# Optimization experiments

Hardware: AMD Instinct MI355X
Metric: run time of the kernel (lower is better)

The kernel has to match this reference:

```python
import jax, jax.numpy as jnp
import numpy as np

B, LT, LM = 4, 2048, 2048
D, F, E, H = 512, 2048, 4, 8
HD = D // H
EPS = 1e-5


def layer_norm(x, g, b):
    mu = jnp.mean(x, axis=-1, keepdims=True)
    var = jnp.mean((x - mu) ** 2, axis=-1, keepdims=True)
    return (x - mu) * jax.lax.rsqrt(var + EPS) * g + b


def mha(q_in, k_in, v_in, in_w, in_b, out_w, out_b):
    # PyTorch nn.MultiheadAttention: packed in_proj [3D, D], out_proj [D, D]
    wq, wk, wv = jnp.split(in_w, 3, axis=0)
    bq, bk, bv = jnp.split(in_b, 3)
    Bq, Lq, _ = q_in.shape
    Lk = k_in.shape[1]
    q = (q_in @ wq.T + bq).reshape(Bq, Lq, H, HD)
    k = (k_in @ wk.T + bk).reshape(Bq, Lk, H, HD)
    v = (v_in @ wv.T + bv).reshape(Bq, Lk, H, HD)
    scale = 1.0 / jnp.sqrt(jnp.asarray(HD, q.dtype))
    attn = jax.nn.softmax(jnp.einsum('bqhd,bkhd->bhqk', q, k) * scale, axis=-1)
    o = jnp.einsum('bhqk,bkhd->bqhd', attn, v).reshape(Bq, Lq, D)
    return o @ out_w.T + out_b


def moe_ff(x, gate_w, gate_b, w1, b1, w2, b2):
    # top_k == 1: argmax routing, mask-and-sum over experts (no score scaling)
    gate_scores = jax.nn.softmax(x @ gate_w.T + gate_b, axis=-1)  # [B,L,E]
    idx = jnp.argmax(gate_scores, axis=-1)                        # [B,L]
    h = jax.nn.gelu(jnp.einsum('bld,edf->eblf', x, w1) + b1[:, None, None, :], approximate=False)
    y = jnp.einsum('eblf,efd->ebld', h, w2) + b2[:, None, None, :]  # [E,B,L,D]
    onehot = jax.nn.one_hot(idx, E, dtype=x.dtype)                  # [B,L,E]
    return jnp.einsum('ebld,ble->bld', y, onehot)


def setup_inputs() -> dict:
    key = jax.random.key(0)
    ks = jax.random.split(key, 20)
    s = 0.02
    n = lambda k, shape: jax.random.normal(k, shape, jnp.float32) * s
    return {
        'x': jax.random.normal(ks[0], (B, LT, D), jnp.float32),
        'memory': jax.random.normal(ks[1], (B, LM, D), jnp.float32),
        'sa_in_w': n(ks[2], (3 * D, D)), 'sa_in_b': n(ks[3], (3 * D,)),
        'sa_out_w': n(ks[4], (D, D)), 'sa_out_b': n(ks[5], (D,)),
        'ca_in_w': n(ks[6], (3 * D, D)), 'ca_in_b': n(ks[7], (3 * D,)),
        'ca_out_w': n(ks[8], (D, D)), 'ca_out_b': n(ks[9], (D,)),
        'gate_w': n(ks[10], (E, D)), 'gate_b': n(ks[11], (E,)),
        'w1': n(ks[12], (E, D, F)), 'b1': n(ks[13], (E, F)),
        'w2': n(ks[14], (E, F, D)), 'b2': n(ks[15], (E, D)),
        'ln1_g': jnp.ones((D,), jnp.float32), 'ln1_b': jnp.zeros((D,), jnp.float32),
        'ln2_g': jnp.ones((D,), jnp.float32), 'ln2_b': jnp.zeros((D,), jnp.float32),
        'ln3_g': jnp.ones((D,), jnp.float32), 'ln3_b': jnp.zeros((D,), jnp.float32),
    }


def reference(x, memory, sa_in_w, sa_in_b, sa_out_w, sa_out_b,
              ca_in_w, ca_in_b, ca_out_w, ca_out_b,
              gate_w, gate_b, w1, b1, w2, b2,
              ln1_g, ln1_b, ln2_g, ln2_b, ln3_g, ln3_b):
    # self-attention + residual + norm (dropout is identity in eval)
    x2 = mha(x, x, x, sa_in_w, sa_in_b, sa_out_w, sa_out_b)
    x = layer_norm(x + x2, ln1_g, ln1_b)
    # cross-attention + residual + norm
    x2 = mha(x, memory, memory, ca_in_w, ca_in_b, ca_out_w, ca_out_b)
    x = layer_norm(x + x2, ln2_g, ln2_b)
    # MoE FFN + residual + norm
    x2 = moe_ff(x, gate_w, gate_b, w1, b1, w2, b2)
    x = layer_norm(x + x2, ln3_g, ln3_b)
    return x
```

## Files before the change

kernel.cpp:

```cpp
#include <hip/hip_runtime.h>

typedef unsigned short u16;
typedef __attribute__((ext_vector_type(8))) short s16x8;
typedef __attribute__((ext_vector_type(8))) unsigned short u16x8;
typedef __attribute__((ext_vector_type(4))) unsigned short u16x4;
typedef __attribute__((ext_vector_type(4))) float f32x4;

#define DEV static __device__ __forceinline__
#define MFMA __builtin_amdgcn_mfma_f32_16x16x32_bf16

DEV float bf2f(u16 u) { return __uint_as_float(((unsigned)u) << 16); }
DEV u16 f2bf(float f) {
    unsigned u = __float_as_uint(f);
    return (u16)((u + 0x7FFFu + ((u >> 16) & 1u)) >> 16);
}
DEV void split2(float v, u16& hi, u16& lo) {
    hi = f2bf(v);
    lo = f2bf(v - bf2f(hi));
}


__global__ __launch_bounds__(256) void split_k(
    const float* __restrict__ src, u16* __restrict__ dh, u16* __restrict__ dl, long n)
{
    const long i = ((long)blockIdx.x * 256 + threadIdx.x) * 8;
    if (i >= n) return;
    float4 f0 = *(const float4*)(src + i);
    float4 f1 = *(const float4*)(src + i + 4);
    float v[8] = {f0.x, f0.y, f0.z, f0.w, f1.x, f1.y, f1.z, f1.w};
    u16x8 h8, l8;
    for (int j = 0; j < 8; ++j) { u16 hh, ll; split2(v[j], hh, ll); h8[j] = hh; l8[j] = ll; }
    *(u16x8*)(dh + i) = h8;
    *(u16x8*)(dl + i) = l8;
}

__global__ __launch_bounds__(256) void splitT_k(
    const float* __restrict__ src, u16* __restrict__ dst, int K, int N)
{
    __shared__ u16 tile[64 * 72];
    const int e = blockIdx.z;
    const int n0 = blockIdx.x * 64, k0 = blockIdx.y * 64;
    const long estride = (long)K * N;
    const int tid = threadIdx.x;
    const int tr = tid >> 2, tc = (tid & 3) * 16;
    {
        const float* sp = src + e * estride + (long)(k0 + tr) * N + n0 + tc;
        for (int j = 0; j < 16; j += 4) {
            float4 f = *(const float4*)(sp + j);
            tile[tr * 72 + tc + j + 0] = f2bf(f.x);
            tile[tr * 72 + tc + j + 1] = f2bf(f.y);
            tile[tr * 72 + tc + j + 2] = f2bf(f.z);
            tile[tr * 72 + tc + j + 3] = f2bf(f.w);
        }
    }
    __syncthreads();
    {
        const int tn = tid >> 2, tk = (tid & 3) * 16;
        u16* dp = dst + e * estride + (long)(n0 + tn) * K + k0 + tk;
        u16x8 o0, o1;
        for (int j = 0; j < 8; ++j) {
            o0[j] = tile[(tk + j) * 72 + tn];
            o1[j] = tile[(tk + 8 + j) * 72 + tn];
        }
        *(u16x8*)(dp) = o0;
        *(u16x8*)(dp + 8) = o1;
    }
}

__global__ __launch_bounds__(256) void gemm_s(
    const float* __restrict__ Af, const u16* __restrict__ Ahp, const u16* __restrict__ Alp,
    int lda, int a_lo, const int* __restrict__ perm_in,
    const u16* __restrict__ Bh, const u16* __restrict__ Bl, int ldb, long b_estride,
    const int* __restrict__ tile_expert,
    const float* __restrict__ bias, int bias_estride,
    float* __restrict__ Cf, int ldcf, const int* __restrict__ perm_out,
    u16* __restrict__ Ch, long clo_off, int ldcp, int ts, long tstride,
    int K, int act)
{
    __shared__ u16 As[64 * 36], Als[64 * 36];
    __shared__ u16 Bs[64 * 36], Bls[64 * 36];
    const int mt = blockIdx.x, nt = blockIdx.y;
    int e = 0;
    if (tile_expert) { e = tile_expert[mt]; if (e < 0) return; }
    const int tid = threadIdx.x, lane = tid & 63, w = tid >> 6;
    const int wr = (w >> 1) * 32, wc = (w & 1) * 32;
    const int quad = lane >> 4, l15 = lane & 15;
    const int b_lo = (Bl != nullptr);

    const u16* Bhb = Bh + (long)e * b_estride;
    const u16* Blb = b_lo ? (Bl + (long)e * b_estride) : nullptr;

    const int r2 = tid >> 3, c4 = (tid & 7) * 4;
    const int r1 = tid >> 2, c8 = (tid & 3) * 8;
    long arow0 = 0, arow1 = 0, arowb = 0;
    bool v0 = true, v1 = true, vb = true;
    if (perm_in) {
        if (Af) {
            int p0 = perm_in[mt * 64 + r2];      v0 = p0 >= 0; arow0 = p0 < 0 ? 0 : p0;
            int p1 = perm_in[mt * 64 + r2 + 32]; v1 = p1 >= 0; arow1 = p1 < 0 ? 0 : p1;
        } else {
            int pb = perm_in[mt * 64 + r1];      vb = pb >= 0; arowb = pb < 0 ? 0 : pb;
        }
    } else {
        arow0 = (long)mt * 64 + r2; arow1 = arow0 + 32; arowb = (long)mt * 64 + r1;
    }

    f32x4 acc[2][2] = {};

    for (int k0 = 0; k0 < K; k0 += 32) {
        __syncthreads();
        if (Af) {
            for (int half = 0; half < 2; ++half) {
                const int row = half * 32 + r2;
                const long ar = half ? arow1 : arow0;
                const bool va = half ? v1 : v0;
                float4 v = va ? *(const float4*)(Af + ar * (long)lda + k0 + c4)
                              : make_float4(0.f, 0.f, 0.f, 0.f);
                float vv[4] = {v.x, v.y, v.z, v.w};
                u16x4 h4, l4;
                for (int i = 0; i < 4; ++i) { u16 hh, ll; split2(vv[i], hh, ll); h4[i] = hh; l4[i] = ll; }
                *(u16x4*)&As[row * 36 + c4] = h4;
                if (a_lo) *(u16x4*)&Als[row * 36 + c4] = l4;
            }
        } else {
            const long ao = arowb * (long)lda + k0 + c8;
            u16x8 h8 = vb ? *(const u16x8*)(Ahp + ao) : (u16x8)(u16)0;
            *(u16x8*)&As[r1 * 36 + c8] = h8;
            if (a_lo) {
                u16x8 l8 = vb ? *(const u16x8*)(Alp + ao) : (u16x8)(u16)0;
                *(u16x8*)&Als[r1 * 36 + c8] = l8;
            }
        }
        {
            const long bo = ((long)nt * 64 + r1) * ldb + k0 + c8;
            *(u16x8*)&Bs[r1 * 36 + c8] = *(const u16x8*)(Bhb + bo);
            if (b_lo) *(u16x8*)&Bls[r1 * 36 + c8] = *(const u16x8*)(Blb + bo);
        }
        __syncthreads();
        s16x8 ah0 = *(const s16x8*)&As[(wr + l15) * 36 + quad * 8];
        s16x8 ah1 = *(const s16x8*)&As[(wr + 16 + l15) * 36 + quad * 8];
        s16x8 bh0 = *(const s16x8*)&Bs[(wc + l15) * 36 + quad * 8];
        s16x8 bh1 = *(const s16x8*)&Bs[(wc + 16 + l15) * 36 + quad * 8];
        acc[0][0] = MFMA(ah0, bh0, acc[0][0], 0, 0, 0);
        acc[0][1] = MFMA(ah0, bh1, acc[0][1], 0, 0, 0);
        acc[1][0] = MFMA(ah1, bh0, acc[1][0], 0, 0, 0);
        acc[1][1] = MFMA(ah1, bh1, acc[1][1], 0, 0, 0);
        if (a_lo) {
            s16x8 al0 = *(const s16x8*)&Als[(wr + l15) * 36 + quad * 8];
            s16x8 al1 = *(const s16x8*)&Als[(wr + 16 + l15) * 36 + quad * 8];
            acc[0][0] = MFMA(al0, bh0, acc[0][0], 0, 0, 0);
            acc[0][1] = MFMA(al0, bh1, acc[0][1], 0, 0, 0);
            acc[1][0] = MFMA(al1, bh0, acc[1][0], 0, 0, 0);
            acc[1][1] = MFMA(al1, bh1, acc[1][1], 0, 0, 0);
        }
        if (b_lo) {
            s16x8 bl0 = *(const s16x8*)&Bls[(wc + l15) * 36 + quad * 8];
            s16x8 bl1 = *(const s16x8*)&Bls[(wc + 16 + l15) * 36 + quad * 8];
            acc[0][0] = MFMA(ah0, bl0, acc[0][0], 0, 0, 0);
            acc[0][1] = MFMA(ah0, bl1, acc[0][1], 0, 0, 0);
            acc[1][0] = MFMA(ah1, bl0, acc[1][0], 0, 0, 0);
            acc[1][1] = MFMA(ah1, bl1, acc[1][1], 0, 0, 0);
        }
    }

    const float* bp = bias + (long)e * bias_estride;
    for (int mi = 0; mi < 2; ++mi) {
        for (int r = 0; r < 4; ++r) {
            const int rloc = wr + mi * 16 + quad * 4 + r;
            const long lrow = (long)mt * 64 + rloc;
            for (int ni = 0; ni < 2; ++ni) {
                const int colg = nt * 64 + wc + ni * 16 + l15;
                float v = acc[mi][ni][r] + bp[colg];
                if (act == 1) v = 0.5f * v * (1.f + erff(v * 0.7071067811865475f));
                if (Cf) {
                    long orow = lrow;
                    if (perm_out) { int po = perm_out[mt * 64 + rloc]; if (po < 0) continue; orow = po; }
                    Cf[orow * (long)ldcf + colg] = v;
                }
                if (Ch) {
                    const int t = colg >> ts;
                    const int cc = colg - (t << ts);
                    const long po = (long)t * tstride + lrow * (long)ldcp + cc;
                    u16 hh, ll; split2(v, hh, ll);
                    Ch[po] = hh;
                    if (clo_off) Ch[po + clo_off] = ll;
                }
            }
        }
    }
}

__global__ __launch_bounds__(256) void attn_p(
    const u16* __restrict__ Qh, const u16* __restrict__ Kh, const u16* __restrict__ Vh,
    long plo, u16* __restrict__ Oh, long olo, int orow_base, float sc)
{
    (void)plo;
    __shared__ u16 Khs[2][64 * 80];
    __shared__ u16 Vhs[2][2][64 * 36];
    const int Z = gridDim.z;
    const int lin = blockIdx.x + 32 * (blockIdx.y + 8 * blockIdx.z);
    const int g = lin & 7, li = lin >> 3;
    const int p = g * Z + (li >> 5);
    const int qt = li & 31;
    const int h = p & 7, z = p >> 3;

    const int tid = threadIdx.x, lane = tid & 63, w = tid >> 6;
    const int quad = lane >> 4, l15 = lane & 15;

    const long qoff = ((long)z * 2048 + qt * 64 + w * 16 + l15) * 512 + h * 64 + quad * 8;
    s16x8 q0, q1;
    {
        s16x8 q0r = *(const s16x8*)(Qh + qoff);
        s16x8 q1r = *(const s16x8*)(Qh + qoff + 32);
        #pragma unroll
        for (int j = 0; j < 8; ++j) {
            q0[j] = (short)f2bf(bf2f((u16)q0r[j]) * sc);
            q1[j] = (short)f2bf(bf2f((u16)q1r[j]) * sc);
        }
    }

    const int kr = tid >> 3, kc = (tid & 7) * 8;
    const int vkey = tid & 31, vhd0 = (tid >> 5) * 8;
    const int vslot = ((vkey >> 2) & 3) * 8 + (vkey & 3) + ((vkey >> 4) << 2);
    const long kbase = ((long)z * 2048 + kr) * 512 + h * 64 + kc;
    const long vbase = ((long)z * 2048 + vkey) * 512 + h * 64 + vhd0;

    {
        u16x8 ka = *(const u16x8*)(Kh + kbase);
        u16x8 kb = *(const u16x8*)(Kh + kbase + 32L * 512);
        u16x8 va = *(const u16x8*)(Vh + vbase);
        u16x8 vb = *(const u16x8*)(Vh + vbase + 32L * 512);
        *(u16x8*)&Khs[0][kr * 80 + kc] = ka;
        *(u16x8*)&Khs[0][(kr + 32) * 80 + kc] = kb;
        #pragma unroll
        for (int i = 0; i < 8; ++i) {
            Vhs[0][0][(vhd0 + i) * 36 + vslot] = va[i];
            Vhs[0][1][(vhd0 + i) * 36 + vslot] = vb[i];
        }
    }

    float l_run = 0.f;
    f32x4 oacc[4] = {};

    for (int t = 0; t < 32; ++t) {
        const int cur = t & 1;
        __syncthreads();
        u16x8 kna, knb, vna, vnb;
        if (t < 31) {
            const long o = (long)(t + 1) * 32768;
            kna = *(const u16x8*)(Kh + kbase + o);
            knb = *(const u16x8*)(Kh + kbase + 32L * 512 + o);
            vna = *(const u16x8*)(Vh + vbase + o);
            vnb = *(const u16x8*)(Vh + vbase + 32L * 512 + o);
        }
        const u16* Kc = Khs[cur];
        f32x4 s0a = {0.f, 0.f, 0.f, 0.f}, s1a = {0.f, 0.f, 0.f, 0.f};
        f32x4 s0b = {0.f, 0.f, 0.f, 0.f}, s1b = {0.f, 0.f, 0.f, 0.f};
        {
            s16x8 a00 = *(const s16x8*)&Kc[l15 * 80 + quad * 8];
            s16x8 a01 = *(const s16x8*)&Kc[l15 * 80 + 32 + quad * 8];
            s16x8 a10 = *(const s16x8*)&Kc[(16 + l15) * 80 + quad * 8];
            s16x8 a11 = *(const s16x8*)&Kc[(16 + l15) * 80 + 32 + quad * 8];
            s16x8 b00 = *(const s16x8*)&Kc[(32 + l15) * 80 + quad * 8];
            s16x8 b01 = *(const s16x8*)&Kc[(32 + l15) * 80 + 32 + quad * 8];
            s16x8 b10 = *(const s16x8*)&Kc[(48 + l15) * 80 + quad * 8];
            s16x8 b11 = *(const s16x8*)&Kc[(48 + l15) * 80 + 32 + quad * 8];
            __builtin_amdgcn_s_setprio(1);
            s0a = MFMA(a00, q0, s0a, 0, 0, 0);
            s1a = MFMA(a10, q0, s1a, 0, 0, 0);
            s0b = MFMA(b00, q0, s0b, 0, 0, 0);
            s1b = MFMA(b10, q0, s1b, 0, 0, 0);
            s0a = MFMA(a01, q1, s0a, 0, 0, 0);
            s1a = MFMA(a11, q1, s1a, 0, 0, 0);
            s0b = MFMA(b01, q1, s0b, 0, 0, 0);
            s1b = MFMA(b11, q1, s1b, 0, 0, 0);
            __builtin_amdgcn_s_setprio(0);
        }
        float pa[8], pb[8];
        pa[0] = exp2f(s0a[0]); pa[1] = exp2f(s0a[1]);
        pa[2] = exp2f(s0a[2]); pa[3] = exp2f(s0a[3]);
        pa[4] = exp2f(s1a[0]); pa[5] = exp2f(s1a[1]);
        pa[6] = exp2f(s1a[2]); pa[7] = exp2f(s1a[3]);
        pb[0] = exp2f(s0b[0]); pb[1] = exp2f(s0b[1]);
        pb[2] = exp2f(s0b[2]); pb[3] = exp2f(s0b[3]);
        pb[4] = exp2f(s1b[0]); pb[5] = exp2f(s1b[1]);
        pb[6] = exp2f(s1b[2]); pb[7] = exp2f(s1b[3]);
        l_run += (((pa[0] + pa[1]) + (pa[2] + pa[3])) +
                  ((pa[4] + pa[5]) + (pa[6] + pa[7]))) +
                 (((pb[0] + pb[1]) + (pb[2] + pb[3])) +
                  ((pb[4] + pb[5]) + (pb[6] + pb[7])));
        s16x8 pha, phb;
        #pragma unroll
        for (int j = 0; j < 8; ++j) {
            pha[j] = (short)(__float_as_uint(pa[j]) >> 16);
            phb[j] = (short)(__float_as_uint(pb[j]) >> 16);
        }
        __builtin_amdgcn_s_setprio(1);
        #pragma unroll
        for (int tt = 0; tt < 4; ++tt) {
            s16x8 vha = *(const s16x8*)&Vhs[cur][0][(tt * 16 + l15) * 36 + quad * 8];
            s16x8 vhb = *(const s16x8*)&Vhs[cur][1][(tt * 16 + l15) * 36 + quad * 8];
            oacc[tt] = MFMA(pha, vha, oacc[tt], 0, 0, 0);
            oacc[tt] = MFMA(phb, vhb, oacc[tt], 0, 0, 0);
        }
        __builtin_amdgcn_s_setprio(0);
        if (t < 31) {
            u16* Kn = (u16*)Khs[cur ^ 1];
            *(u16x8*)&Kn[kr * 80 + kc] = kna;
            *(u16x8*)&Kn[(kr + 32) * 80 + kc] = knb;
            #pragma unroll
            for (int i = 0; i < 8; ++i) {
                Vhs[cur ^ 1][0][(vhd0 + i) * 36 + vslot] = vna[i];
                Vhs[cur ^ 1][1][(vhd0 + i) * 36 + vslot] = vnb[i];
            }
        }
    }

    l_run += __shfl_xor(l_run, 16);
    l_run += __shfl_xor(l_run, 32);
    float linv[4];
    #pragma unroll
    for (int r = 0; r < 4; ++r)
        linv[r] = 1.f / fmaxf(__shfl(l_run, quad * 4 + r), 1e-35f);
    const long obase = ((long)orow_base + z * 2048 + qt * 64 + w * 16 + quad * 4) * 512 + h * 64;
    for (int tt = 0; tt < 4; ++tt)
        for (int r = 0; r < 4; ++r) {
            u16 hh, ll; split2(oacc[tt][r] * linv[r], hh, ll);
            const long oo = obase + (long)r * 512 + tt * 16 + l15;
            Oh[oo] = hh;
            Oh[olo + oo] = ll;
        }
}

__global__ __launch_bounds__(256) void ln_p(
    const float* __restrict__ af, const u16* __restrict__ ah, long alo,
    const float* __restrict__ bf, const u16* __restrict__ bh, long blo,
    const float* __restrict__ g, const float* __restrict__ be,
    float* __restrict__ of, u16* __restrict__ oh, long olo)
{
    const int tid = threadIdx.x, lane = tid & 63, w = tid >> 6;
    const long base = ((long)blockIdx.x * 4 + w) * 512 + lane * 8;
    float v[8];
    if (af) {
        float4 f0 = *(const float4*)(af + base);
        float4 f1 = *(const float4*)(af + base + 4);
        v[0] = f0.x; v[1] = f0.y; v[2] = f0.z; v[3] = f0.w;
        v[4] = f1.x; v[5] = f1.y; v[6] = f1.z; v[7] = f1.w;
    } else {
        u16x8 hh = *(const u16x8*)(ah + base);
        u16x8 ll = *(const u16x8*)(ah + alo + base);
        for (int j = 0; j < 8; ++j) v[j] = bf2f(hh[j]) + bf2f(ll[j]);
    }
    if (bf) {
        float4 f0 = *(const float4*)(bf + base);
        float4 f1 = *(const float4*)(bf + base + 4);
        v[0] += f0.x; v[1] += f0.y; v[2] += f0.z; v[3] += f0.w;
        v[4] += f1.x; v[5] += f1.y; v[6] += f1.z; v[7] += f1.w;
    } else {
        u16x8 hh = *(const u16x8*)(bh + base);
        u16x8 ll = *(const u16x8*)(bh + blo + base);
        for (int j = 0; j < 8; ++j) v[j] += bf2f(hh[j]) + bf2f(ll[j]);
    }
    float s = 0.f, sq = 0.f;
    for (int j = 0; j < 8; ++j) { s += v[j]; sq += v[j] * v[j]; }
    for (int m = 1; m < 64; m <<= 1) { s += __shfl_xor(s, m); sq += __shfl_xor(sq, m); }
    const float mu = s * (1.f / 512.f);
    const float var = fmaxf(sq * (1.f / 512.f) - mu * mu, 0.f);
    const float rs = rsqrtf(var + 1e-5f);
    float4 ga = *(const float4*)(g + lane * 8);
    float4 gb = *(const float4*)(g + lane * 8 + 4);
    float4 ba = *(const float4*)(be + lane * 8);
    float4 bb = *(const float4*)(be + lane * 8 + 4);
    float gg[8] = {ga.x, ga.y, ga.z, ga.w, gb.x, gb.y, gb.z, gb.w};
    float bv[8] = {ba.x, ba.y, ba.z, ba.w, bb.x, bb.y, bb.z, bb.w};
    float o[8];
    for (int j = 0; j < 8; ++j) o[j] = (v[j] - mu) * rs * gg[j] + bv[j];
    if (of) {
        *(float4*)(of + base)     = make_float4(o[0], o[1], o[2], o[3]);
        *(float4*)(of + base + 4) = make_float4(o[4], o[5], o[6], o[7]);
    }
    if (oh) {
        u16x8 h8, l8;
        for (int j = 0; j < 8; ++j) { u16 hh, ll; split2(o[j], hh, ll); h8[j] = hh; l8[j] = ll; }
        *(u16x8*)(oh + base) = h8;
        *(u16x8*)(oh + olo + base) = l8;
    }
}

__global__ __launch_bounds__(256) void route_p(
    const u16* __restrict__ xh, long xlo,
    const float* __restrict__ gw, const float* __restrict__ gb,
    int* __restrict__ idx)
{
    const int tid = threadIdx.x, lane = tid & 63, w = tid >> 6;
    const long row = (long)blockIdx.x * 4 + w;
    const long base = row * 512 + lane * 8;
    u16x8 hh = *(const u16x8*)(xh + base);
    u16x8 ll = *(const u16x8*)(xh + xlo + base);
    float xf[8];
    for (int j = 0; j < 8; ++j) xf[j] = bf2f(hh[j]) + bf2f(ll[j]);
    float d0 = 0.f, d1 = 0.f, d2 = 0.f, d3 = 0.f;
    {
        float4 w0 = *(const float4*)(gw + 0 * 512 + lane * 8);
        float4 w1 = *(const float4*)(gw + 0 * 512 + lane * 8 + 4);
        float wf[8] = {w0.x, w0.y, w0.z, w0.w, w1.x, w1.y, w1.z, w1.w};
        for (int j = 0; j < 8; ++j) d0 += xf[j] * wf[j];
    }
    {
        float4 w0 = *(const float4*)(gw + 1 * 512 + lane * 8);
        float4 w1 = *(const float4*)(gw + 1 * 512 + lane * 8 + 4);
        float wf[8] = {w0.x, w0.y, w0.z, w0.w, w1.x, w1.y, w1.z, w1.w};
        for (int j = 0; j < 8; ++j) d1 += xf[j] * wf[j];
    }
    {
        float4 w0 = *(const float4*)(gw + 2 * 512 + lane * 8);
        float4 w1 = *(const float4*)(gw + 2 * 512 + lane * 8 + 4);
        float wf[8] = {w0.x, w0.y, w0.z, w0.w, w1.x, w1.y, w1.z, w1.w};
        for (int j = 0; j < 8; ++j) d2 += xf[j] * wf[j];
    }
    {
        float4 w0 = *(const float4*)(gw + 3 * 512 + lane * 8);
        float4 w1 = *(const float4*)(gw + 3 * 512 + lane * 8 + 4);
        float wf[8] = {w0.x, w0.y, w0.z, w0.w, w1.x, w1.y, w1.z, w1.w};
        for (int j = 0; j < 8; ++j) d3 += xf[j] * wf[j];
    }
    for (int m = 1; m < 64; m <<= 1) {
        d0 += __shfl_xor(d0, m);
        d1 += __shfl_xor(d1, m);
        d2 += __shfl_xor(d2, m);
        d3 += __shfl_xor(d3, m);
    }
    if (lane == 0) {
        d0 += gb[0]; d1 += gb[1]; d2 += gb[2]; d3 += gb[3];
        float best = d0; int bi = 0;
        if (d1 > best) { best = d1; bi = 1; }
        if (d2 > best) { best = d2; bi = 2; }
        if (d3 > best) { best = d3; bi = 3; }
        idx[row] = bi;
    }
}

__global__ void plan_k(const int* __restrict__ idx, int* __restrict__ cursors,
                       int* __restrict__ tile_expert)
{
    int c0 = 0, c1 = 0, c2 = 0, c3 = 0;
    for (int i = threadIdx.x; i < 8192; i += 64) {
        const int e = idx[i];
        c0 += (e == 0); c1 += (e == 1); c2 += (e == 2); c3 += (e == 3);
    }
    for (int m = 1; m < 64; m <<= 1) {
        c0 += __shfl_xor(c0, m);
        c1 += __shfl_xor(c1, m);
        c2 += __shfl_xor(c2, m);
        c3 += __shfl_xor(c3, m);
    }
    if (threadIdx.x == 0) {
        int counts[4] = {c0, c1, c2, c3};
        int off = 0;
        for (int e = 0; e < 4; ++e) {
            cursors[e] = off;
            int nt = (counts[e] + 63) >> 6;
            int t0 = off >> 6;
            for (int i = 0; i < nt; ++i) tile_expert[t0 + i] = e;
            off += nt << 6;
        }
        for (int t = off >> 6; t < 132; ++t) tile_expert[t] = -1;
    }
}

__global__ __launch_bounds__(256) void scatter_k(
    const int* __restrict__ idx, int* __restrict__ cursors, int* __restrict__ perm)
{
    __shared__ int lcnt[4];
    __shared__ int lbase[4];
    const int t = blockIdx.x * 256 + threadIdx.x;
    if (threadIdx.x < 4) lcnt[threadIdx.x] = 0;
    __syncthreads();
    const int e = idx[t];
    const int lr = atomicAdd(&lcnt[e], 1);
    __syncthreads();
    if (threadIdx.x < 4)
        lbase[threadIdx.x] = atomicAdd(&cursors[threadIdx.x], lcnt[threadIdx.x]);
    __syncthreads();
    perm[lbase[e] + lr] = t;
}

extern "C" void kernel_launch(void* const* d_in, const int* in_sizes, int n_in,
                              void* d_out, int out_size, void* d_ws, size_t ws_size,
                              hipStream_t stream)
{
    (void)in_sizes; (void)n_in; (void)out_size;
    const float* x        = (const float*)d_in[0];
    const float* mem      = (const float*)d_in[1];
    const float* sa_in_w  = (const float*)d_in[2];
    const float* sa_in_b  = (const float*)d_in[3];
    const float* sa_out_w = (const float*)d_in[4];
    const float* sa_out_b = (const float*)d_in[5];
    const float* ca_in_w  = (const float*)d_in[6];
    const float* ca_in_b  = (const float*)d_in[7];
    const float* ca_out_w = (const float*)d_in[8];
    const float* ca_out_b = (const float*)d_in[9];
    const float* gate_w   = (const float*)d_in[10];
    const float* gate_b   = (const float*)d_in[11];
    const float* w1       = (const float*)d_in[12];
    const float* b1       = (const float*)d_in[13];
    const float* w2       = (const float*)d_in[14];
    const float* b2       = (const float*)d_in[15];
    const float* ln1_g    = (const float*)d_in[16];
    const float* ln1_b    = (const float*)d_in[17];
    const float* ln2_g    = (const float*)d_in[18];
    const float* ln2_b    = (const float*)d_in[19];
    const float* ln3_g    = (const float*)d_in[20];
    const float* ln3_b    = (const float*)d_in[21];

    const float sc = 0.125f * 1.4426950408889634f;
    dim3 blk(256, 1, 1);
    char* ws = (char*)d_ws;

    const long WAe_sa_in = 0, WAe_sa_out = 1572864, WAe_ca_in = 2097152, WAe_ca_out = 3670016;

    const size_t BIG_NEED  = 109119104;
    const size_t FAST_NEED = 100730416;

    if (ws_size >= BIG_NEED) {
        u16* WA   = (u16*)(ws);
        u16* QKVp = (u16*)(ws + 8388608L);
        u16* Op   = (u16*)(ws + 58720256L);
        float* ymoe = (float*)(ws + 58720256L);
        u16* P1p  = (u16*)(ws + 75497472L);
        u16* X1p  = (u16*)(ws + 92274688L);
        int* idx    = (int*)(ws + 109051904L);
        int* perm   = (int*)(ws + 109051904L + 32768);
        int* counts = (int*)(ws + 109051904L + 32768 + 33792);
        int* cursors= (int*)(ws + 109051904L + 32768 + 33792 + 16);
        int* tile_e = (int*)(ws + 109051904L + 32768 + 33792 + 32);
        (void)counts;

        const long L = 4194304;
        const long T = 8388608;

        hipMemsetAsync(perm, 0xFF, 8448 * 4, stream);

        split_k<<<dim3(384), blk, 0, stream>>>(sa_in_w,  WA + WAe_sa_in,  WA + WAe_sa_in + 786432, 786432);
        split_k<<<dim3(128), blk, 0, stream>>>(sa_out_w, WA + WAe_sa_out, WA + WAe_sa_out + 262144, 262144);
        split_k<<<dim3(384), blk, 0, stream>>>(ca_in_w,  WA + WAe_ca_in,  WA + WAe_ca_in + 786432, 786432);
        split_k<<<dim3(128), blk, 0, stream>>>(ca_out_w, WA + WAe_ca_out, WA + WAe_ca_out + 262144, 262144);

        gemm_s<<<dim3(128, 24), blk, 0, stream>>>(
            x, nullptr, nullptr, 512, 0, nullptr,
            WA + WAe_sa_in, nullptr, 512, 0, nullptr,
            sa_in_b, 0, nullptr, 0, nullptr,
            QKVp, 0, 512, 9, T, 512, 0);
        attn_p<<<dim3(32, 8, 4), blk, 0, stream>>>(
            QKVp, QKVp + T, QKVp + 2 * T, L, Op, L, 0, sc);
        gemm_s<<<dim3(128, 8), blk, 0, stream>>>(
            nullptr, Op, Op + L, 512, 1, nullptr,
            WA + WAe_sa_out, WA + WAe_sa_out + 262144, 512, 0, nullptr,
            sa_out_b, 0, nullptr, 0, nullptr,
            P1p, L, 512, 9, 0, 512, 0);
        ln_p<<<dim3(2048), blk, 0, stream>>>(x, nullptr, 0, nullptr, P1p, L,
                                             ln1_g, ln1_b, nullptr, X1p, L);

        gemm_s<<<dim3(128, 8), blk, 0, stream>>>(
            nullptr, X1p, nullptr, 512, 0, nullptr,
            WA + WAe_ca_in, nullptr, 512, 0, nullptr,
            ca_in_b, 0, nullptr, 0, nullptr,
            QKVp, 0, 512, 9, T, 512, 0);
        gemm_s<<<dim3(128, 16), blk, 0, stream>>>(
            mem, nullptr, nullptr, 512, 0, nullptr,
            WA + WAe_ca_in + 262144, nullptr, 512, 0, nullptr,
            ca_in_b + 512, 0, nullptr, 0, nullptr,
            QKVp + T, 0, 512, 9, T, 512, 0);
        attn_p<<<dim3(32, 8, 4), blk, 0, stream>>>(
            QKVp, QKVp + T, QKVp + 2 * T, L, Op, L, 0, sc);
        gemm_s<<<dim3(128, 8), blk, 0, stream>>>(
            nullptr, Op, Op + L, 512, 1, nullptr,
            WA + WAe_ca_out, WA + WAe_ca_out + 262144, 512, 0, nullptr,
            ca_out_b, 0, nullptr, 0, nullptr,
            P1p, L, 512, 9, 0, 512, 0);
        ln_p<<<dim3(2048), blk, 0, stream>>>(nullptr, X1p, L, nullptr, P1p, L,
                                             ln2_g, ln2_b, nullptr, X1p, L);

        route_p<<<dim3(2048), blk, 0, stream>>>(X1p, L, gate_w, gate_b, idx);
        plan_k<<<dim3(1), dim3(64), 0, stream>>>(idx, cursors, tile_e);
        scatter_k<<<dim3(32), blk, 0, stream>>>(idx, cursors, perm);
        splitT_k<<<dim3(32, 8, 4), blk, 0, stream>>>(w1, P1p, 512, 2048);
        splitT_k<<<dim3(8, 32, 4), blk, 0, stream>>>(w2, P1p + 4194304, 2048, 512);
        gemm_s<<<dim3(132, 32), blk, 0, stream>>>(
            nullptr, X1p, nullptr, 512, 0, perm,
            P1p, nullptr, 512, 1048576, tile_e,
            b1, 2048, nullptr, 0, nullptr,
            QKVp, 0, 2048, 31, 0, 512, 1);
        gemm_s<<<dim3(132, 8), blk, 0, stream>>>(
            nullptr, QKVp, nullptr, 2048, 0, nullptr,
            P1p + 4194304, nullptr, 2048, 1048576, tile_e,
            b2, 512, ymoe, 512, perm,
            nullptr, 0, 0, 31, 0, 2048, 0);
        ln_p<<<dim3(2048), blk, 0, stream>>>(nullptr, X1p, L, ymoe, nullptr, 0,
                                             ln3_g, ln3_b, (float*)d_out, nullptr, 0);
    } else {
        u16* WA   = (u16*)(ws);
        u16* w1h  = (u16*)(ws + 8388608L);
        u16* w2h  = (u16*)(ws + 16777216L);
        u16* QKVp = (u16*)(ws + 25165824L);
        u16* Op   = (u16*)(ws + 50331648L);
        u16* P1p  = (u16*)(ws + 67108864L);
        float* ymoe = (float*)(ws + 67108864L);
        u16* X1p  = (u16*)(ws + 83886080L);
        int* idx    = (int*)(ws + 100663296L);
        int* perm   = (int*)(ws + 100663296L + 32768);
        int* counts = (int*)(ws + 100663296L + 32768 + 33792);
        int* cursors= (int*)(ws + 100663296L + 32768 + 33792 + 16);
        int* tile_e = (int*)(ws + 100663296L + 32768 + 33792 + 32);
        (void)counts;

        const long L_QKV = 2097152, T_QKV = 4194304, L_8K = 4194304;
        const long SL = 1048576;

        hipMemsetAsync(perm, 0xFF, 8448 * 4, stream);

        split_k<<<dim3(384), blk, 0, stream>>>(sa_in_w,  WA + WAe_sa_in,  WA + WAe_sa_in + 786432, 786432);
        split_k<<<dim3(128), blk, 0, stream>>>(sa_out_w, WA + WAe_sa_out, WA + WAe_sa_out + 262144, 262144);
        split_k<<<dim3(384), blk, 0, stream>>>(ca_in_w,  WA + WAe_ca_in,  WA + WAe_ca_in + 786432, 786432);
        split_k<<<dim3(128), blk, 0, stream>>>(ca_out_w, WA + WAe_ca_out, WA + WAe_ca_out + 262144, 262144);
        splitT_k<<<dim3(32, 8, 4), blk, 0, stream>>>(w1, w1h, 512, 2048);
        splitT_k<<<dim3(8, 32, 4), blk, 0, stream>>>(w2, w2h, 2048, 512);

        for (int hB = 0; hB < 2; ++hB) {
            gemm_s<<<dim3(64, 24), blk, 0, stream>>>(
                x + hB * 2 * SL, nullptr, nullptr, 512, 0, nullptr,
                WA + WAe_sa_in, nullptr, 512, 0, nullptr,
                sa_in_b, 0, nullptr, 0, nullptr,
                QKVp, 0, 512, 9, T_QKV, 512, 0);
            attn_p<<<dim3(32, 8, 2), blk, 0, stream>>>(
                QKVp, QKVp + T_QKV, QKVp + 2 * T_QKV, L_QKV, Op, L_8K, hB * 4096, sc);
        }
        gemm_s<<<dim3(128, 8), blk, 0, stream>>>(
            nullptr, Op, Op + L_8K, 512, 1, nullptr,
            WA + WAe_sa_out, WA + WAe_sa_out + 262144, 512, 0, nullptr,
            sa_out_b, 0, nullptr, 0, nullptr,
            P1p, L_8K, 512, 9, 0, 512, 0);
        ln_p<<<dim3(2048), blk, 0, stream>>>(x, nullptr, 0, nullptr, P1p, L_8K,
                                             ln1_g, ln1_b, nullptr, X1p, L_8K);

        for (int hB = 0; hB < 2; ++hB) {
            gemm_s<<<dim3(64, 8), blk, 0, stream>>>(
                nullptr, X1p + hB * L_QKV, nullptr, 512, 0, nullptr,
                WA + WAe_ca_in, nullptr, 512, 0, nullptr,
                ca_in_b, 0, nullptr, 0, nullptr,
                QKVp, 0, 512, 9, T_QKV, 512, 0);
            gemm_s<<<dim3(64, 16), blk, 0, stream>>>(
                mem + hB * 2 * SL, nullptr, nullptr, 512, 0, nullptr,
                WA + WAe_ca_in + 262144, nullptr, 512, 0, nullptr,
                ca_in_b + 512, 0, nullptr, 0, nullptr,
                QKVp + T_QKV, 0, 512, 9, T_QKV, 512, 0);
            attn_p<<<dim3(32, 8, 2), blk, 0, stream>>>(
                QKVp, QKVp + T_QKV, QKVp + 2 * T_QKV, L_QKV, Op, L_8K, hB * 4096, sc);
        }
        gemm_s<<<dim3(128, 8), blk, 0, stream>>>(
            nullptr, Op, Op + L_8K, 512, 1, nullptr,
            WA + WAe_ca_out, WA + WAe_ca_out + 262144, 512, 0, nullptr,
            ca_out_b, 0, nullptr, 0, nullptr,
            P1p, L_8K, 512, 9, 0, 512, 0);
        ln_p<<<dim3(2048), blk, 0, stream>>>(nullptr, X1p, L_8K, nullptr, P1p, L_8K,
                                             ln2_g, ln2_b, nullptr, X1p, L_8K);

        route_p<<<dim3(2048), blk, 0, stream>>>(X1p, L_8K, gate_w, gate_b, idx);
        plan_k<<<dim3(1), dim3(64), 0, stream>>>(idx, cursors, tile_e);
        scatter_k<<<dim3(32), blk, 0, stream>>>(idx, cursors, perm);
        for (int c = 0; c < 2; ++c) {
            const int t0 = c * 66;
            gemm_s<<<dim3(66, 32), blk, 0, stream>>>(
                nullptr, X1p, nullptr, 512, 0, perm + t0 * 64,
                w1h, nullptr, 512, 1048576, tile_e + t0,
                b1, 2048, nullptr, 0, nullptr,
                QKVp, 0, 2048, 31, 0, 512, 1);
            gemm_s<<<dim3(66, 8), blk, 0, stream>>>(
                nullptr, QKVp, nullptr, 2048, 0, nullptr,
                w2h, nullptr, 2048, 1048576, tile_e + t0,
                b2, 512, ymoe, 512, perm + t0 * 64,
                nullptr, 0, 0, 31, 0, 2048, 0);
        }
        ln_p<<<dim3(2048), blk, 0, stream>>>(nullptr, X1p, L_8K, ymoe, nullptr, 0,
                                             ln3_g, ln3_b, (float*)d_out, nullptr, 0);
    }
}
```

Before: 647.3 us.

## Unify workspace paths into single full-batch schedule with hi-only QKV buffers

Removes the workspace-size branch and always uses the compact workspace layout. The separate w1h/w2h weight buffers are kept, and self- and cross-attention now run over the full batch in one launch instead of two half-batch chunks. The attention kernel's Q/K/V low-part offset is passed as 0, so attention appears to consume only a single bf16 component rather than a hi/lo split. This is meant to cut launch count and QKV memory traffic, at the risk of lower attention precision and of the MoE GEMMs staying split into two chunks.

```diff
diff --git a/kernel.cpp b/kernel.cpp
--- a/kernel.cpp
+++ b/kernel.cpp
@@ -489,7 +489,7 @@
                               void* d_out, int out_size, void* d_ws, size_t ws_size,
                               hipStream_t stream)
 {
-    (void)in_sizes; (void)n_in; (void)out_size;
+    (void)in_sizes; (void)n_in; (void)out_size; (void)ws_size;
     const float* x        = (const float*)d_in[0];
     const float* mem      = (const float*)d_in[1];
     const float* sa_in_w  = (const float*)d_in[2];
@@ -519,169 +519,84 @@
 
     const long WAe_sa_in = 0, WAe_sa_out = 1572864, WAe_ca_in = 2097152, WAe_ca_out = 3670016;
 
-    const size_t BIG_NEED  = 109119104;
-    const size_t FAST_NEED = 100730416;
-
-    if (ws_size >= BIG_NEED) {
-        u16* WA   = (u16*)(ws);
-        u16* QKVp = (u16*)(ws + 8388608L);
-        u16* Op   = (u16*)(ws + 58720256L);
-        float* ymoe = (float*)(ws + 58720256L);
-        u16* P1p  = (u16*)(ws + 75497472L);
-        u16* X1p  = (u16*)(ws + 92274688L);
-        int* idx    = (int*)(ws + 109051904L);
-        int* perm   = (int*)(ws + 109051904L + 32768);
-        int* counts = (int*)(ws + 109051904L + 32768 + 33792);
-        int* cursors= (int*)(ws + 109051904L + 32768 + 33792 + 16);
-        int* tile_e = (int*)(ws + 109051904L + 32768 + 33792 + 32);
-        (void)counts;
-
-        const long L = 4194304;
-        const long T = 8388608;
-
-        hipMemsetAsync(perm, 0xFF, 8448 * 4, stream);
-
-        split_k<<<dim3(384), blk, 0, stream>>>(sa_in_w,  WA + WAe_sa_in,  WA + WAe_sa_in + 786432, 786432);
-        split_k<<<dim3(128), blk, 0, stream>>>(sa_out_w, WA + WAe_sa_out, WA + WAe_sa_out + 262144, 262144);
-        split_k<<<dim3(384), blk, 0, stream>>>(ca_in_w,  WA + WAe_ca_in,  WA + WAe_ca_in + 786432, 786432);
-        split_k<<<dim3(128), blk, 0, stream>>>(ca_out_w, WA + WAe_ca_out, WA + WAe_ca_out + 262144, 262144);
-
-        gemm_s<<<dim3(128, 24), blk, 0, stream>>>(
-            x, nullptr, nullptr, 512, 0, nullptr,
-            WA + WAe_sa_in, nullptr, 512, 0, nullptr,
-            sa_in_b, 0, nullptr, 0, nullptr,
-            QKVp, 0, 512, 9, T, 512, 0);
-        attn_p<<<dim3(32, 8, 4), blk, 0, stream>>>(
-            QKVp, QKVp + T, QKVp + 2 * T, L, Op, L, 0, sc);
-        gemm_s<<<dim3(128, 8), blk, 0, stream>>>(
-            nullptr, Op, Op + L, 512, 1, nullptr,
-            WA + WAe_sa_out, WA + WAe_sa_out + 262144, 512, 0, nullptr,
-            sa_out_b, 0, nullptr, 0, nullptr,
-            P1p, L, 512, 9, 0, 512, 0);
-        ln_p<<<dim3(2048), blk, 0, stream>>>(x, nullptr, 0, nullptr, P1p, L,
-                                             ln1_g, ln1_b, nullptr, X1p, L);
-
-        gemm_s<<<dim3(128, 8), blk, 0, stream>>>(
-            nullptr, X1p, nullptr, 512, 0, nullptr,
-            WA + WAe_ca_in, nullptr, 512, 0, nullptr,
-            ca_in_b, 0, nullptr, 0, nullptr,
-            QKVp, 0, 512, 9, T, 512, 0);
-        gemm_s<<<dim3(128, 16), blk, 0, stream>>>(
-            mem, nullptr, nullptr, 512, 0, nullptr,
-            WA + WAe_ca_in + 262144, nullptr, 512, 0, nullptr,
-            ca_in_b + 512, 0, nullptr, 0, nullptr,
-            QKVp + T, 0, 512, 9, T, 512, 0);
-        attn_p<<<dim3(32, 8, 4), blk, 0, stream>>>(
-            QKVp, QKVp + T, QKVp + 2 * T, L, Op, L, 0, sc);
-        gemm_s<<<dim3(128, 8), blk, 0, stream>>>(
-            nullptr, Op, Op + L, 512, 1, nullptr,
-            WA + WAe_ca_out, WA + WAe_ca_out + 262144, 512, 0, nullptr,
-            ca_out_b, 0, nullptr, 0, nullptr,
-            P1p, L, 512, 9, 0, 512, 0);
-        ln_p<<<dim3(2048), blk, 0, stream>>>(nullptr, X1p, L, nullptr, P1p, L,
-                                             ln2_g, ln2_b, nullptr, X1p, L);
-
-        route_p<<<dim3(2048), blk, 0, stream>>>(X1p, L, gate_w, gate_b, idx);
-        plan_k<<<dim3(1), dim3(64), 0, stream>>>(idx, cursors, tile_e);
-        scatter_k<<<dim3(32), blk, 0, stream>>>(idx, cursors, perm);
-        splitT_k<<<dim3(32, 8, 4), blk, 0, stream>>>(w1, P1p, 512, 2048);
-        splitT_k<<<dim3(8, 32, 4), blk, 0, stream>>>(w2, P1p + 4194304, 2048, 512);
-        gemm_s<<<dim3(132, 32), blk, 0, stream>>>(
-            nullptr, X1p, nullptr, 512, 0, perm,
-            P1p, nullptr, 512, 1048576, tile_e,
+    u16* WA   = (u16*)(ws);
+    u16* w1h  = (u16*)(ws + 8388608L);
+    u16* w2h  = (u16*)(ws + 16777216L);
+    u16* QKVp = (u16*)(ws + 25165824L);
+    u16* Op   = (u16*)(ws + 50331648L);
+    u16* P1p  = (u16*)(ws + 67108864L);
+    float* ymoe = (float*)(ws + 67108864L);
+    u16* X1p  = (u16*)(ws + 83886080L);
+    int* idx    = (int*)(ws + 100663296L);
+    int* perm   = (int*)(ws + 100663296L + 32768);
+    int* cursors= (int*)(ws + 100663296L + 32768 + 33792 + 16);
+    int* tile_e = (int*)(ws + 100663296L + 32768 + 33792 + 32);
+
+    const long T    = 4194304;
+    const long L_8K = 4194304;
+    const long SL   = 1048576;
+    (void)SL;
+
+    hipMemsetAsync(perm, 0xFF, 8448 * 4, stream);
+
+    split_k<<<dim3(384), blk, 0, stream>>>(sa_in_w,  WA + WAe_sa_in,  WA + WAe_sa_in + 786432, 786432);
+    split_k<<<dim3(128), blk, 0, stream>>>(sa_out_w, WA + WAe_sa_out, WA + WAe_sa_out + 262144, 262144);
+    split_k<<<dim3(384), blk, 0, stream>>>(ca_in_w,  WA + WAe_ca_in,  WA + WAe_ca_in + 786432, 786432);
+    split_k<<<dim3(128), blk, 0, stream>>>(ca_out_w, WA + WAe_ca_out, WA + WAe_ca_out + 262144, 262144);
+    splitT_k<<<dim3(32, 8, 4), blk, 0, stream>>>(w1, w1h, 512, 2048);
+    splitT_k<<<dim3(8, 32, 4), blk, 0, stream>>>(w2, w2h, 2048, 512);
+
+    gemm_s<<<dim3(128, 24), blk, 0, stream>>>(
+        x, nullptr, nullptr, 512, 0, nullptr,
+        WA + WAe_sa_in, nullptr, 512, 0, nullptr,
+        sa_in_b, 0, nullptr, 0, nullptr,
+        QKVp, 0, 512, 9, T, 512, 0);
+    attn_p<<<dim3(32, 8, 4), blk, 0, stream>>>(
+        QKVp, QKVp + T, QKVp + 2 * T, 0, Op, L_8K, 0, sc);
+    gemm_s<<<dim3(128, 8), blk, 0, stream>>>(
+        nullptr, Op, Op + L_8K, 512, 1, nullptr,
+        WA + WAe_sa_out, WA + WAe_sa_out + 262144, 512, 0, nullptr,
+        sa_out_b, 0, nullptr, 0, nullptr,
+        P1p, L_8K, 512, 9, 0, 512, 0);
+    ln_p<<<dim3(2048), blk, 0, stream>>>(x, nullptr, 0, nullptr, P1p, L_8K,
+                                         ln1_g, ln1_b, nullptr, X1p, L_8K);
+
+    gemm_s<<<dim3(128, 8), blk, 0, stream>>>(
+        nullptr, X1p, nullptr, 512, 0, nullptr,
+        WA + WAe_ca_in, nullptr, 512, 0, nullptr,
+        ca_in_b, 0, nullptr, 0, nullptr,
+        QKVp, 0, 512, 9, T, 512, 0);
+    gemm_s<<<dim3(128, 16), blk, 0, stream>>>(
+        mem, nullptr, nullptr, 512, 0, nullptr,
+        WA + WAe_ca_in + 262144, nullptr, 512, 0, nullptr,
+        ca_in_b + 512, 0, nullptr, 0, nullptr,
+        QKVp + T, 0, 512, 9, T, 512, 0);
+    attn_p<<<dim3(32, 8, 4), blk, 0, stream>>>(
+        QKVp, QKVp + T, QKVp + 2 * T, 0, Op, L_8K, 0, sc);
+    gemm_s<<<dim3(128, 8), blk, 0, stream>>>(
+        nullptr, Op, Op + L_8K, 512, 1, nullptr,
+        WA + WAe_ca_out, WA + WAe_ca_out + 262144, 512, 0, nullptr,
+        ca_out_b, 0, nullptr, 0, nullptr,
+        P1p, L_8K, 512, 9, 0, 512, 0);
+    ln_p<<<dim3(2048), blk, 0, stream>>>(nullptr, X1p, L_8K, nullptr, P1p, L_8K,
+                                         ln2_g, ln2_b, nullptr, X1p, L_8K);
+
+    route_p<<<dim3(2048), blk, 0, stream>>>(X1p, L_8K, gate_w, gate_b, idx);
+    plan_k<<<dim3(1), dim3(64), 0, stream>>>(idx, cursors, tile_e);
+    scatter_k<<<dim3(32), blk, 0, stream>>>(idx, cursors, perm);
+    for (int c = 0; c < 2; ++c) {
+        const int t0 = c * 66;
+        gemm_s<<<dim3(66, 32), blk, 0, stream>>>(
+            nullptr, X1p, nullptr, 512, 0, perm + t0 * 64,
+            w1h, nullptr, 512, 1048576, tile_e + t0,
             b1, 2048, nullptr, 0, nullptr,
             QKVp, 0, 2048, 31, 0, 512, 1);
-        gemm_s<<<dim3(132, 8), blk, 0, stream>>>(
+        gemm_s<<<dim3(66, 8), blk, 0, stream>>>(
             nullptr, QKVp, nullptr, 2048, 0, nullptr,
-            P1p + 4194304, nullptr, 2048, 1048576, tile_e,
-            b2, 512, ymoe, 512, perm,
+            w2h, nullptr, 2048, 1048576, tile_e + t0,
+            b2, 512, ymoe, 512, perm + t0 * 64,
             nullptr, 0, 0, 31, 0, 2048, 0);
-        ln_p<<<dim3(2048), blk, 0, stream>>>(nullptr, X1p, L, ymoe, nullptr, 0,
-                                             ln3_g, ln3_b, (float*)d_out, nullptr, 0);
-    } else {
-        u16* WA   = (u16*)(ws);
-        u16* w1h  = (u16*)(ws + 8388608L);
-        u16* w2h  = (u16*)(ws + 16777216L);
-        u16* QKVp = (u16*)(ws + 25165824L);
-        u16* Op   = (u16*)(ws + 50331648L);
-        u16* P1p  = (u16*)(ws + 67108864L);
-        float* ymoe = (float*)(ws + 67108864L);
-        u16* X1p  = (u16*)(ws + 83886080L);
-        int* idx    = (int*)(ws + 100663296L);
-        int* perm   = (int*)(ws + 100663296L + 32768);
-        int* counts = (int*)(ws + 100663296L + 32768 + 33792);
-        int* cursors= (int*)(ws + 100663296L + 32768 + 33792 + 16);
-        int* tile_e = (int*)(ws + 100663296L + 32768 + 33792 + 32);
-        (void)counts;
-
-        const long L_QKV = 2097152, T_QKV = 4194304, L_8K = 4194304;
-        const long SL = 1048576;
-
-        hipMemsetAsync(perm, 0xFF, 8448 * 4, stream);
-
-        split_k<<<dim3(384), blk, 0, stream>>>(sa_in_w,  WA + WAe_sa_in,  WA + WAe_sa_in + 786432, 786432);
-        split_k<<<dim3(128), blk, 0, stream>>>(sa_out_w, WA + WAe_sa_out, WA + WAe_sa_out + 262144, 262144);
-        split_k<<<dim3(384), blk, 0, stream>>>(ca_in_w,  WA + WAe_ca_in,  WA + WAe_ca_in + 786432, 786432);
-        split_k<<<dim3(128), blk, 0, stream>>>(ca_out_w, WA + WAe_ca_out, WA + WAe_ca_out + 262144, 262144);
-        splitT_k<<<dim3(32, 8, 4), blk, 0, stream>>>(w1, w1h, 512, 2048);
-        splitT_k<<<dim3(8, 32, 4), blk, 0, stream>>>(w2, w2h, 2048, 512);
-
-        for (int hB = 0; hB < 2; ++hB) {
-            gemm_s<<<dim3(64, 24), blk, 0, stream>>>(
-                x + hB * 2 * SL, nullptr, nullptr, 512, 0, nullptr,
-                WA + WAe_sa_in, nullptr, 512, 0, nullptr,
-                sa_in_b, 0, nullptr, 0, nullptr,
-                QKVp, 0, 512, 9, T_QKV, 512, 0);
-            attn_p<<<dim3(32, 8, 2), blk, 0, stream>>>(
-                QKVp, QKVp + T_QKV, QKVp + 2 * T_QKV, L_QKV, Op, L_8K, hB * 4096, sc);
-        }
-        gemm_s<<<dim3(128, 8), blk, 0, stream>>>(
-            nullptr, Op, Op + L_8K, 512, 1, nullptr,
-            WA + WAe_sa_out, WA + WAe_sa_out + 262144, 512, 0, nullptr,
-            sa_out_b, 0, nullptr, 0, nullptr,
-            P1p, L_8K, 512, 9, 0, 512, 0);
-        ln_p<<<dim3(2048), blk, 0, stream>>>(x, nullptr, 0, nullptr, P1p, L_8K,
-                                             ln1_g, ln1_b, nullptr, X1p, L_8K);
-
-        for (int hB = 0; hB < 2; ++hB) {
-            gemm_s<<<dim3(64, 8), blk, 0, stream>>>(
-                nullptr, X1p + hB * L_QKV, nullptr, 512, 0, nullptr,
-                WA + WAe_ca_in, nullptr, 512, 0, nullptr,
-                ca_in_b, 0, nullptr, 0, nullptr,
-                QKVp, 0, 512, 9, T_QKV, 512, 0);
-            gemm_s<<<dim3(64, 16), blk, 0, stream>>>(
-                mem + hB * 2 * SL, nullptr, nullptr, 512, 0, nullptr,
-                WA + WAe_ca_in + 262144, nullptr, 512, 0, nullptr,
-                ca_in_b + 512, 0, nullptr, 0, nullptr,
-                QKVp + T_QKV, 0, 512, 9, T_QKV, 512, 0);
-            attn_p<<<dim3(32, 8, 2), blk, 0, stream>>>(
-                QKVp, QKVp + T_QKV, QKVp + 2 * T_QKV, L_QKV, Op, L_8K, hB * 4096, sc);
-        }
-        gemm_s<<<dim3(128, 8), blk, 0, stream>>>(
-            nullptr, Op, Op + L_8K, 512, 1, nullptr,
-            WA + WAe_ca_out, WA + WAe_ca_out + 262144, 512, 0, nullptr,
-            ca_out_b, 0, nullptr, 0, nullptr,
-            P1p, L_8K, 512, 9, 0, 512, 0);
-        ln_p<<<dim3(2048), blk, 0, stream>>>(nullptr, X1p, L_8K, nullptr, P1p, L_8K,
-                                             ln2_g, ln2_b, nullptr, X1p, L_8K);
-
-        route_p<<<dim3(2048), blk, 0, stream>>>(X1p, L_8K, gate_w, gate_b, idx);
-        plan_k<<<dim3(1), dim3(64), 0, stream>>>(idx, cursors, tile_e);
-        scatter_k<<<dim3(32), blk, 0, stream>>>(idx, cursors, perm);
-        for (int c = 0; c < 2; ++c) {
-            const int t0 = c * 66;
-            gemm_s<<<dim3(66, 32), blk, 0, stream>>>(
-                nullptr, X1p, nullptr, 512, 0, perm + t0 * 64,
-                w1h, nullptr, 512, 1048576, tile_e + t0,
-                b1, 2048, nullptr, 0, nullptr,
-                QKVp, 0, 2048, 31, 0, 512, 1);
-            gemm_s<<<dim3(66, 8), blk, 0, stream>>>(
-                nullptr, QKVp, nullptr, 2048, 0, nullptr,
-                w2h, nullptr, 2048, 1048576, tile_e + t0,
-                b2, 512, ymoe, 512, perm + t0 * 64,
-                nullptr, 0, 0, 31, 0, 2048, 0);
-        }
-        ln_p<<<dim3(2048), blk, 0, stream>>>(nullptr, X1p, L_8K, ymoe, nullptr, 0,
-                                             ln3_g, ln3_b, (float*)d_out, nullptr, 0);
-    }
-}
+    }
+    ln_p<<<dim3(2048), blk, 0, stream>>>(nullptr, X1p, L_8K, ymoe, nullptr, 0,
+                                         ln3_g, ln3_b, (float*)d_out, nullptr, 0);
+}
```

Result: slower. 696.4 us (+7.6%).
